# Kernel optimization log

Hardware: AMD Instinct MI355X
Metric: run time of the kernel (lower is better)

## Reference

```python
import jax, jax.numpy as jnp
import numpy as np
import math

PS = 8  # patch size (hard-coded in module)
DEPTH = 6
LAMBDA_INIT = 0.8 - 0.6 * math.exp(-0.3 * DEPTH)

# torch_dct norm=None DCT-II matrix: y_k = 2 * sum_n x_n cos(pi*(2n+1)k/(2N))
_n = np.arange(PS)
_C = 2.0 * np.cos(np.pi * (2 * _n[None, :] + 1) * _n[:, None] / (2 * PS))  # [k, n]
_Ci = np.linalg.inv(_C)
DCT_M = jnp.asarray(_C, jnp.float32)
IDCT_M = jnp.asarray(_Ci, jnp.float32)


def dct2(x):  # 2D DCT over last two dims (torch_dct.dct_2d, norm=None)
    return jnp.einsum('...mn,am,bn->...ab', x, DCT_M, DCT_M)


def idct2(x):  # exact inverse (torch_dct.idct_2d, norm=None)
    return jnp.einsum('...ab,ma,nb->...mn', x, IDCT_M, IDCT_M)


def conv1x1(x, w):  # w: [O, I]
    return jnp.einsum('oi,bihw->bohw', w, x)


def dw3(x, w):  # depthwise 3x3, stride 1, pad 1; w: [C, 1, 3, 3]
    return jax.lax.conv_general_dilated(
        x, w, window_strides=(1, 1), padding='SAME',
        dimension_numbers=('NCHW', 'OIHW', 'NCHW'),
        feature_group_count=x.shape[1])


def prelu(t, a):
    return jnp.where(t >= 0, t, a * t)


def setup_inputs() -> dict:
    key = jax.random.key(0)
    ks = jax.random.split(key, 20)
    b, c, H, W = 2, 64, 384, 384
    w = lambda k, shape: jax.random.normal(k, shape, jnp.float32) * 0.05
    heads = c // 16
    return {
        'x': jax.random.normal(ks[0], (b, c, H, W), jnp.float32),
        'nir': jax.random.normal(ks[1], (b, c, H, W), jnp.float32),
        'w_hidden': w(ks[2], (c, c)),
        'w_hidden_nir': w(ks[3], (2 * c, c)),
        'w_dw': w(ks[4], (c, 1, 3, 3)),
        'w_dw_nir': w(ks[5], (2 * c, 1, 3, 3)),
        'temperature': jnp.ones((heads, 1, 1), jnp.float32),
        'w_proj_mid': w(ks[6], (c, c)),
        'w_proj_out': w(ks[7], (c, c)),
        'w_p1a': w(ks[8], (c, 1, 3, 3)),
        'a_p1': jnp.asarray(0.25, jnp.float32),
        'w_p1b': w(ks[9], (c, 1, 3, 3)),
        'w_p2a': w(ks[10], (c, 1, 3, 3)),
        'a_p2': jnp.asarray(0.25, jnp.float32),
        'w_p2b': w(ks[11], (c, 1, 3, 3)),
        'lq1': jax.random.normal(ks[12], (c,), jnp.float32) * 0.1,
        'lk1': jax.random.normal(ks[13], (c,), jnp.float32) * 0.1,
        'lq2': jax.random.normal(ks[14], (c,), jnp.float32) * 0.1,
        'lk2': jax.random.normal(ks[15], (c,), jnp.float32) * 0.1,
    }


def reference(x, nir, w_hidden, w_hidden_nir, w_dw, w_dw_nir, temperature,
              w_proj_mid, w_proj_out, w_p1a, a_p1, w_p1b, w_p2a, a_p2, w_p2b,
              lq1, lk1, lq2, lk2):
    b, c, H, W = x.shape
    heads = c // 16
    hh, ww = H // PS, W // PS

    hidden = conv1x1(x, w_hidden)
    nir_hidden = conv1x1(nir, w_hidden_nir)
    q = dw3(hidden, w_dw)
    kv = dw3(nir_hidden, w_dw_nir)
    k, v = kv[:, :c], kv[:, c:]

    # b c (hh p1) (ww p2) -> b c hh ww p1 p2
    patch = lambda t: t.reshape(b, c, hh, PS, ww, PS).transpose(0, 1, 2, 4, 3, 5)
    q_fft = dct2(patch(q))
    k_fft = dct2(patch(k))
    out1 = q_fft * k_fft

    L = hh * ww * PS * PS
    hf = lambda t: t.reshape(b, heads, c // heads, L)  # b head c L
    q_fft, k_fft, out1f = hf(q_fft), hf(k_fft), hf(out1)

    qn = q_fft / jnp.maximum(jnp.linalg.norm(q_fft, axis=-1, keepdims=True), 1e-12)
    kn = k_fft / jnp.maximum(jnp.linalg.norm(k_fft, axis=-1, keepdims=True), 1e-12)

    attn = jax.nn.softmax(jnp.einsum('bhcl,bhdl->bhcd', qn, kn) * temperature, axis=-1)
    o = jnp.einsum('bhcd,bhdl->bhcl', attn, out1f)

    o = o.reshape(b, c, hh, ww, PS, PS)
    o = idct2(o)
    o = o.transpose(0, 1, 2, 4, 3, 5).reshape(b, c, H, W)
    out = conv1x1(o, w_proj_mid)

    lam1 = jnp.exp(jnp.sum(lq1 * lk1))
    lam2 = jnp.exp(jnp.sum(lq2 * lk2))
    lam = lam1 - lam2 + LAMBDA_INIT

    pool = lambda t, wa, a, wb: dw3(prelu(dw3(t, wa), a), wb)
    output = pool(q * out, w_p1a, a_p1, w_p1b) + pool(v - lam * (v * out), w_p2a, a_p2, w_p2b)
    return conv1x1(output, w_proj_out)
```

## Files before the change

kernel.cpp:

```cpp
#include <hip/hip_runtime.h>
#include <cmath>

#ifndef M_PI
#define M_PI 3.14159265358979323846
#endif

#define NB      2
#define N_PIX   147456
#define L_LEN   147456
#define TENS_SZ ((long)NB * 64 * N_PIX)

#define OFF_C    0
#define OFF_CI   64
#define OFF_LAM  128
#define OFF_GRAM 256
#define OFF_QQ   2304
#define OFF_KK   2432
#define OFF_ATTN 2560

#define TW 128
#define TH 16
#define LW 136
#define LH 18
#define PLH 20

__global__ __launch_bounds__(64) void init_k(const float* __restrict__ lq1, const float* __restrict__ lk1,
                                             const float* __restrict__ lq2, const float* __restrict__ lk2,
                                             float* __restrict__ sm) {
  int t = threadIdx.x;
  int a = t >> 3, m = t & 7;
  double cv = 2.0 * cos(M_PI * (double)((2 * m + 1) * a) / 16.0);
  sm[OFF_C + a * 8 + m] = (float)cv;
  sm[OFF_CI + m * 8 + a] = (float)(cv / ((a == 0) ? 32.0 : 16.0));
  float p1 = lq1[t] * lk1[t];
  float p2 = lq2[t] * lk2[t];
  #pragma unroll
  for (int off = 32; off; off >>= 1) {
    p1 += __shfl_xor(p1, off, 64);
    p2 += __shfl_xor(p2, off, 64);
  }
  if (t == 0) sm[OFF_LAM] = expf(p1) - expf(p2) + 0.70082066706704813f;
  for (int i = t; i < 2304; i += 64) sm[OFF_GRAM + i] = 0.f;
}

__global__ void diag_k(float* out, float v) { out[0] = v; }

__global__ __launch_bounds__(256) void conv1x1_k(const float* __restrict__ in, const float* __restrict__ w,
                                                 float* __restrict__ out) {
  __shared__ float ws[4096];
  int t = threadIdx.x;
  for (int j = t; j < 1024; j += 256)
    *reinterpret_cast<float4*>(ws + j * 4) = *reinterpret_cast<const float4*>(w + j * 4);
  __syncthreads();

  long gp = (long)blockIdx.x * 256;
  int bb = (int)(gp / N_PIX);
  int p0 = (int)(gp - (long)bb * N_PIX);
  int lane = t & 63;
  int co0 = (t >> 6) * 16;

  const float* ip = in + (long)bb * 64 * N_PIX + p0 + lane * 4;
  const float* wp = ws + co0 * 64;

  float acc[16][4];
  #pragma unroll
  for (int j = 0; j < 16; j++)
    #pragma unroll
    for (int p = 0; p < 4; p++) acc[j][p] = 0.f;

  for (int c4 = 0; c4 < 16; c4++) {
    float4 x0 = *reinterpret_cast<const float4*>(ip + (long)(c4 * 4 + 0) * N_PIX);
    float4 x1 = *reinterpret_cast<const float4*>(ip + (long)(c4 * 4 + 1) * N_PIX);
    float4 x2 = *reinterpret_cast<const float4*>(ip + (long)(c4 * 4 + 2) * N_PIX);
    float4 x3 = *reinterpret_cast<const float4*>(ip + (long)(c4 * 4 + 3) * N_PIX);
    #pragma unroll
    for (int j = 0; j < 16; j++) {
      float4 w4 = *reinterpret_cast<const float4*>(wp + j * 64 + c4 * 4);
// ... 41 lines not shown
    __syncthreads();
    const float* wp = ws + co0 * 64;
    float acc[16][4];
    #pragma unroll
    for (int j = 0; j < 16; j++)
      #pragma unroll
      for (int p = 0; p < 4; p++) acc[j][p] = 0.f;
    for (int c4 = 0; c4 < 16; c4++) {
      float4 x0 = *reinterpret_cast<const float4*>(ip + (long)(c4 * 4 + 0) * N_PIX);
      float4 x1 = *reinterpret_cast<const float4*>(ip + (long)(c4 * 4 + 1) * N_PIX);
      float4 x2 = *reinterpret_cast<const float4*>(ip + (long)(c4 * 4 + 2) * N_PIX);
      float4 x3 = *reinterpret_cast<const float4*>(ip + (long)(c4 * 4 + 3) * N_PIX);
      #pragma unroll
      for (int j = 0; j < 16; j++) {
        float4 w4 = *reinterpret_cast<const float4*>(wp + j * 64 + c4 * 4);
        acc[j][0] = fmaf(w4.x, x0.x, acc[j][0]);
        acc[j][0] = fmaf(w4.y, x1.x, acc[j][0]);
        acc[j][0] = fmaf(w4.z, x2.x, acc[j][0]);
        acc[j][0] = fmaf(w4.w, x3.x, acc[j][0]);
        acc[j][1] = fmaf(w4.x, x0.y, acc[j][1]);
        acc[j][1] = fmaf(w4.y, x1.y, acc[j][1]);
        acc[j][1] = fmaf(w4.z, x2.y, acc[j][1]);
        acc[j][1] = fmaf(w4.w, x3.y, acc[j][1]);
        acc[j][2] = fmaf(w4.x, x0.z, acc[j][2]);
        acc[j][2] = fmaf(w4.y, x1.z, acc[j][2]);
        acc[j][2] = fmaf(w4.z, x2.z, acc[j][2]);
        acc[j][2] = fmaf(w4.w, x3.z, acc[j][2]);
        acc[j][3] = fmaf(w4.x, x0.w, acc[j][3]);
        acc[j][3] = fmaf(w4.y, x1.w, acc[j][3]);
        acc[j][3] = fmaf(w4.z, x2.w, acc[j][3]);
        acc[j][3] = fmaf(w4.w, x3.w, acc[j][3]);
      }
    }
    float* op = (half ? outv : outk) + (long)bb * 64 * N_PIX + p0 + lane * 4;
    #pragma unroll
    for (int j = 0; j < 16; j++)
      *reinterpret_cast<float4*>(op + (long)(co0 + j) * N_PIX) =
          make_float4(acc[j][0], acc[j][1], acc[j][2], acc[j][3]);
  }
}

__device__ __forceinline__ float4 load_g4(const float* __restrict__ p, int gy, int gx) {
  if ((unsigned)gy >= 384u) return make_float4(0.f, 0.f, 0.f, 0.f);
  if (gx >= 0 && gx + 3 < 384) return *reinterpret_cast<const float4*>(p + gy * 384 + gx);
  float e[4];
  #pragma unroll
  for (int i = 0; i < 4; i++) {
    int xx = gx + i;
    e[i] = ((unsigned)xx < 384u) ? p[gy * 384 + xx] : 0.f;
  }
  return make_float4(e[0], e[1], e[2], e[3]);
}

__global__ __launch_bounds__(256) void dw3t_k(const float* __restrict__ in, const float* __restrict__ w,
                                              float* __restrict__ out) {
  __shared__ float sT[LH * LW];
  int plane = blockIdx.z;
  int ch = plane & 63;
  int x0 = blockIdx.x * TW, y0 = blockIdx.y * TH;
  const float* ip = in + (long)plane * N_PIX;
  int t = threadIdx.x;
  for (int j = t; j < LH * 34; j += 256) {
    int row = j / 34, c4 = j - row * 34;
    *reinterpret_cast<float4*>(sT + row * LW + c4 * 4) = load_g4(ip, y0 - 1 + row, x0 - 4 + c4 * 4);
  }
  __syncthreads();
  const float* wp = w + ch * 9;
  float w00 = wp[0], w01 = wp[1], w02 = wp[2];
  float w10 = wp[3], w11 = wp[4], w12 = wp[5];
  float w20 = wp[6], w21 = wp[7], w22 = wp[8];
  int col = t & 127, rg = t >> 7;
  int lc = col + 4;
  int r0 = rg * 8;
  float a0 = sT[r0 * LW + lc - 1],       a1 = sT[r0 * LW + lc],       a2 = sT[r0 * LW + lc + 1];
  float b0 = sT[(r0 + 1) * LW + lc - 1], b1 = sT[(r0 + 1) * LW + lc], b2 = sT[(r0 + 1) * LW + lc + 1];
  float* op = out + (long)plane * N_PIX + (long)(y0 + rg * 8) * 384 + x0 + col;
  #pragma unroll
  for (int i = 0; i < 8; i++) {
    int lr = r0 + i + 2;
    float c0 = sT[lr * LW + lc - 1], c1 = sT[lr * LW + lc], c2 = sT[lr * LW + lc + 1];
    float s = w00 * a0;
    s = fmaf(w01, a1, s); s = fmaf(w02, a2, s);
    s = fmaf(w10, b0, s); s = fmaf(w11, b1, s); s = fmaf(w12, b2, s);
    s = fmaf(w20, c0, s); s = fmaf(w21, c1, s); s = fmaf(w22, c2, s);
    op[i * 384] = s;
    a0 = b0; a1 = b1; a2 = b2;
    b0 = c0; b1 = c1; b2 = c2;
  }
}

__global__ __launch_bounds__(256) void dw3dct_k(const float* __restrict__ in, const float* __restrict__ w,
                                                const float* __restrict__ sm,
                                                float* __restrict__ outf, float* __restrict__ outs) {
  __shared__ float sT[LH * LW];
  __shared__ float Cm[64];
  int t = threadIdx.x;
  if (t < 64) Cm[t] = sm[OFF_C + t];
  int plane = blockIdx.z;
  int ch = plane & 63;
  int x0 = blockIdx.x * TW, y0 = blockIdx.y * TH;
  const float* ip = in + (long)plane * N_PIX;
  for (int j = t; j < LH * 34; j += 256) {
    int row = j / 34, c4 = j - row * 34;
    *reinterpret_cast<float4*>(sT + row * LW + c4 * 4) = load_g4(ip, y0 - 1 + row, x0 - 4 + c4 * 4);
  }
  __syncthreads();
  const float* wp = w + ch * 9;
  float w00 = wp[0], w01 = wp[1], w02 = wp[2];
  float w10 = wp[3], w11 = wp[4], w12 = wp[5];
  float w20 = wp[6], w21 = wp[7], w22 = wp[8];
  int col = t & 127, rg = t >> 7;
  int lc = col + 4;
  int r0 = rg * 8;
  float r[8];
  {
    float a0 = sT[r0 * LW + lc - 1],       a1 = sT[r0 * LW + lc],       a2 = sT[r0 * LW + lc + 1];
    float b0 = sT[(r0 + 1) * LW + lc - 1], b1 = sT[(r0 + 1) * LW + lc], b2 = sT[(r0 + 1) * LW + lc + 1];
    #pragma unroll
    for (int i = 0; i < 8; i++) {
      int lr = r0 + i + 2;
      float c0 = sT[lr * LW + lc - 1], c1 = sT[lr * LW + lc], c2 = sT[lr * LW + lc + 1];
      float s = w00 * a0;
      s = fmaf(w01, a1, s); s = fmaf(w02, a2, s);
      s = fmaf(w10, b0, s); s = fmaf(w11, b1, s); s = fmaf(w12, b2, s);
      s = fmaf(w20, c0, s); s = fmaf(w21, c1, s); s = fmaf(w22, c2, s);
      r[i] = s;
      a0 = b0; a1 = b1; a2 = b2;
      b0 = c0; b1 = c1; b2 = c2;
    }
  }
  if (outs) {
    float* op = outs + (long)plane * N_PIX + (long)(y0 + r0) * 384 + x0 + col;
    #pragma unroll
    for (int i = 0; i < 8; i++) op[i * 384] = r[i];
  }
  __syncthreads();
  #pragma unroll
  for (int i = 0; i < 8; i++) sT[(r0 + i + 1) * LW + lc] = r[i];
  __syncthreads();
  int patch = t >> 3, a = t & 7;
  int prow = patch >> 4, pcol = patch & 15;
  const float* xb = sT + (prow * 8 + 1) * LW + pcol * 8 + 4;
  float T[8];
  #pragma unroll
  for (int n = 0; n < 8; n++) {
    float s = 0.f;
    #pragma unroll
    for (int m = 0; m < 8; m++) s = fmaf(Cm[a * 8 + m], xb[m * LW + n], s);
    T[n] = s;
  }
  float o[8];
  #pragma unroll
  for (int b8 = 0; b8 < 8; b8++) {
    float s = 0.f;
    #pragma unroll
    for (int n = 0; n < 8; n++) s = fmaf(Cm[b8 * 8 + n], T[n], s);
    o[b8] = s;
  }
  int py = (y0 >> 3) + prow, px = (x0 >> 3) + pcol;
  float* op = outf + (long)plane * L_LEN + (long)(py * 48 + px) * 64 + a * 8;
  *reinterpret_cast<float4*>(op)     = make_float4(o[0], o[1], o[2], o[3]);
  *reinterpret_cast<float4*>(op + 4) = make_float4(o[4], o[5], o[6], o[7]);
}

__device__ __forceinline__ void stencil_col9(const float* __restrict__ sb, int ci, int rs0,
                                             float w00, float w01, float w02,
                                             float w10, float w11, float w12,
                                             float w20, float w21, float w22,
                                             float alpha, bool xok, int y0,
                                             float* __restrict__ r) {
  float a0 = sb[rs0 * LW + ci - 1],       a1 = sb[rs0 * LW + ci],       a2 = sb[rs0 * LW + ci + 1];
  float b0 = sb[(rs0 + 1) * LW + ci - 1], b1 = sb[(rs0 + 1) * LW + ci], b2 = sb[(rs0 + 1) * LW + ci + 1];
  #pragma unroll
  for (int ii = 0; ii < 9; ii++) {
    int rs2 = rs0 + ii + 2;
    float c0 = sb[rs2 * LW + ci - 1], c1 = sb[rs2 * LW + ci], c2 = sb[rs2 * LW + ci + 1];
    float s = w00 * a0;
    s = fmaf(w01, a1, s); s = fmaf(w02, a2, s);
    s = fmaf(w10, b0, s); s = fmaf(w11, b1, s); s = fmaf(w12, b2, s);
    s = fmaf(w20, c0, s); s = fmaf(w21, c1, s); s = fmaf(w22, c2, s);
    s = (s >= 0.f) ? s : alpha * s;
    int gy = y0 - 1 + rs0 + ii;
    r[ii] = (xok && (unsigned)gy < 384u) ? s : 0.f;
    a0 = b0; a1 = b1; a2 = b2;
    b0 = c0; b1 = c1; b2 = c2;
  }
}

__global__ __launch_bounds__(256) void pool_k(const float* __restrict__ q, const float* __restrict__ om,
                                              const float* __restrict__ v,
                                              const float* __restrict__ w1a, const float* __restrict__ a1p,
                                              const float* __restrict__ w1b,
                                              const float* __restrict__ w2a, const float* __restrict__ a2p,
                                              const float* __restrict__ w2b,
                                              const float* __restrict__ sm,
                                              float* __restrict__ outp) {
  __shared__ float s1[PLH * LW], s2[PLH * LW];
  int plane = blockIdx.z;
  int ch = plane & 63;
  int x0 = blockIdx.x * TW, y0 = blockIdx.y * TH;
  const float* qp = q  + (long)plane * N_PIX;
  const float* op = om + (long)plane * N_PIX;
  const float* vp = v  + (long)plane * N_PIX;
  float lam = sm[OFF_LAM];
  int t = threadIdx.x;
  for (int j = t; j < PLH * 34; j += 256) {
    int row = j / 34, c4 = j - row * 34;
    int gy = y0 - 2 + row, gx = x0 - 4 + c4 * 4;
    float4 qv = load_g4(qp, gy, gx);
    float4 ov = load_g4(op, gy, gx);
    float4 vv = load_g4(vp, gy, gx);
    *reinterpret_cast<float4*>(s1 + row * LW + c4 * 4) =
        make_float4(qv.x * ov.x, qv.y * ov.y, qv.z * ov.z, qv.w * ov.w);
    *reinterpret_cast<float4*>(s2 + row * LW + c4 * 4) =
        make_float4(vv.x - lam * vv.x * ov.x, vv.y - lam * vv.y * ov.y,
                    vv.z - lam * vv.z * ov.z, vv.w - lam * vv.w * ov.w);
  }
  __syncthreads();

  int ct = t & 127, rg = t >> 7;
  int rs0 = rg * 9;
  int ci0 = 3 + ct;
  int ci1 = 131 + ct;
  bool xok0 = (unsigned)(x0 - 4 + ci0) < 384u;
  bool xok1 = (unsigned)(x0 - 4 + ci1) < 384u;

  {
    const float* wp1 = w1a + ch * 9;
    float w00 = wp1[0], w01 = wp1[1], w02 = wp1[2], w10 = wp1[3], w11 = wp1[4],
          w12 = wp1[5], w20 = wp1[6], w21 = wp1[7], w22 = wp1[8];
    float alpha = a1p[0];
    float rm[9], re[9];
    stencil_col9(s1, ci0, rs0, w00, w01, w02, w10, w11, w12, w20, w21, w22, alpha, xok0, y0, rm);
    if (ct < 2)
      stencil_col9(s1, ci1, rs0, w00, w01, w02, w10, w11, w12, w20, w21, w22, alpha, xok1, y0, re);
    __syncthreads();
    #pragma unroll
    for (int ii = 0; ii < 9; ii++) s1[(rs0 + ii + 1) * LW + ci0] = rm[ii];
    if (ct < 2) {
      #pragma unroll
      for (int ii = 0; ii < 9; ii++) s1[(rs0 + ii + 1) * LW + ci1] = re[ii];
    }
  }
  {
    const float* wp2 = w2a + ch * 9;
    float w00 = wp2[0], w01 = wp2[1], w02 = wp2[2], w10 = wp2[3], w11 = wp2[4],
          w12 = wp2[5], w20 = wp2[6], w21 = wp2[7], w22 = wp2[8];
    float alpha = a2p[0];
    float rm[9], re[9];
    stencil_col9(s2, ci0, rs0, w00, w01, w02, w10, w11, w12, w20, w21, w22, alpha, xok0, y0, rm);
    if (ct < 2)
      stencil_col9(s2, ci1, rs0, w00, w01, w02, w10, w11, w12, w20, w21, w22, alpha, xok1, y0, re);
    __syncthreads();
    #pragma unroll
    for (int ii = 0; ii < 9; ii++) s2[(rs0 + ii + 1) * LW + ci0] = rm[ii];
    if (ct < 2) {
      #pragma unroll
      for (int ii = 0; ii < 9; ii++) s2[(rs0 + ii + 1) * LW + ci1] = re[ii];
    }
  }
  __syncthreads();
  {
    const float* wp1 = w1b + ch * 9;
    const float* wp2 = w2b + ch * 9;
    float p00 = wp1[0], p01 = wp1[1], p02 = wp1[2], p10 = wp1[3], p11 = wp1[4], p12 = wp1[5], p20 = wp1[6], p21 = wp1[7], p22 = wp1[8];
    float q00 = wp2[0], q01 = wp2[1], q02 = wp2[2], q10 = wp2[3], q11 = wp2[4], q12 = wp2[5], q20 = wp2[6], q21 = wp2[7], q22 = wp2[8];
    int col = t & 127, rg2 = t >> 7;
    int lc = col + 4;
    int rb = rg2 * 8 + 1;
    float xa0 = s1[rb * LW + lc - 1],       xa1 = s1[rb * LW + lc],       xa2 = s1[rb * LW + lc + 1];
    float xb0 = s1[(rb + 1) * LW + lc - 1], xb1 = s1[(rb + 1) * LW + lc], xb2 = s1[(rb + 1) * LW + lc + 1];
    float ya0 = s2[rb * LW + lc - 1],       ya1 = s2[rb * LW + lc],       ya2 = s2[rb * LW + lc + 1];
    float yb0 = s2[(rb + 1) * LW + lc - 1], yb1 = s2[(rb + 1) * LW + lc], yb2 = s2[(rb + 1) * LW + lc + 1];
    float* wo = outp + (long)plane * N_PIX + (long)(y0 + rg2 * 8) * 384 + x0 + col;
    #pragma unroll
    for (int i = 0; i < 8; i++) {
      int lr = rb + i + 2;
      float xc0 = s1[lr * LW + lc - 1], xc1 = s1[lr * LW + lc], xc2 = s1[lr * LW + lc + 1];
      float yc0 = s2[lr * LW + lc - 1], yc1 = s2[lr * LW + lc], yc2 = s2[lr * LW + lc + 1];
      float s = p00 * xa0;
      s = fmaf(p01, xa1, s); s = fmaf(p02, xa2, s);
      s = fmaf(p10, xb0, s); s = fmaf(p11, xb1, s); s = fmaf(p12, xb2, s);
      s = fmaf(p20, xc0, s); s = fmaf(p21, xc1, s); s = fmaf(p22, xc2, s);
      s = fmaf(q00, ya0, s); s = fmaf(q01, ya1, s); s = fmaf(q02, ya2, s);
      s = fmaf(q10, yb0, s); s = fmaf(q11, yb1, s); s = fmaf(q12, yb2, s);
      s = fmaf(q20, yc0, s); s = fmaf(q21, yc1, s); s = fmaf(q22, yc2, s);
      wo[i * 384] = s;
      xa0 = xb0; xa1 = xb1; xa2 = xb2; xb0 = xc0; xb1 = xc1; xb2 = xc2;
      ya0 = yb0; ya1 = yb1; ya2 = yb2; yb0 = yc0; yb1 = yc1; yb2 = yc2;
    }
  }
}

__global__ __launch_bounds__(256) void dct_k(const float* __restrict__ in,
                                             const float* __restrict__ sm, float* __restrict__ outf) {
  __shared__ float Cm[64];
  if (threadIdx.x < 64) Cm[threadIdx.x] = sm[OFF_C + threadIdx.x];
  __syncthreads();
  int pid = blockIdx.x * 256 + threadIdx.x;
  int wx = pid % 48;
  int t1 = pid / 48;
  int hy = t1 % 48; t1 /= 48;
  int ch = t1 & 63;
  int bb = t1 >> 6;
  const float* ip = in + (long)(bb * 64 + ch) * N_PIX + (hy * 8) * 384 + wx * 8;
  float X[8][8];
  #pragma unroll
  for (int r = 0; r < 8; r++) {
    float4 v0 = *reinterpret_cast<const float4*>(ip + r * 384);
    float4 v1 = *reinterpret_cast<const float4*>(ip + r * 384 + 4);
    X[r][0] = v0.x; X[r][1] = v0.y; X[r][2] = v0.z; X[r][3] = v0.w;
    X[r][4] = v1.x; X[r][5] = v1.y; X[r][6] = v1.z; X[r][7] = v1.w;
  }
  float T[8][8];
  #pragma unroll
  for (int a = 0; a < 8; a++)
    #pragma unroll
    for (int n = 0; n < 8; n++) {
      float s = 0.f;
      #pragma unroll
      for (int m = 0; m < 8; m++) s = fmaf(Cm[a * 8 + m], X[m][n], s);
      T[a][n] = s;
    }
  #pragma unroll
  for (int a = 0; a < 8; a++)
    #pragma unroll
    for (int b8 = 0; b8 < 8; b8++) {
      float s = 0.f;
      #pragma unroll
      for (int n = 0; n < 8; n++) s = fmaf(Cm[b8 * 8 + n], T[a][n], s);
      X[a][b8] = s;
    }
  float* op = outf + (long)(bb * 64 + ch) * L_LEN + (long)(hy * 48 + wx) * 64;
  float4* o4 = reinterpret_cast<float4*>(op);
  #pragma unroll
  for (int a = 0; a < 8; a++) {
    o4[a * 2]     = make_float4(X[a][0], X[a][1], X[a][2], X[a][3]);
    o4[a * 2 + 1] = make_float4(X[a][4], X[a][5], X[a][6], X[a][7]);
  }
}

#define GS_P 132
__global__ __launch_bounds__(256) void gram_k(const float* __restrict__ qf, const float* __restrict__ kf,
                                              float* __restrict__ sm) {
  __shared__ float qs[16 * GS_P], ks[16 * GS_P];
  int t = threadIdx.x;
  int bh = blockIdx.y;
  int bb = bh >> 2, h = bh & 3;
  const float* qbase = qf + ((long)bb * 64 + h * 16) * L_LEN;
  const float* kbase = kf + ((long)bb * 64 + h * 16) * L_LEN;
  int c = t >> 4, d = t & 15;
  long l0 = (long)blockIdx.x * 2048;
  float g = 0.f, nq = 0.f, nk = 0.f;
  for (int chunk = 0; chunk < 16; chunk++) {
    long lc = l0 + chunk * 128;
    __syncthreads();
    for (int j = t; j < 512; j += 256) {
      int row = j >> 5, c4 = j & 31;
      *reinterpret_cast<float4*>(qs + row * GS_P + c4 * 4) =
          *reinterpret_cast<const float4*>(qbase + (long)row * L_LEN + lc + c4 * 4);
      *reinterpret_cast<float4*>(ks + row * GS_P + c4 * 4) =
          *reinterpret_cast<const float4*>(kbase + (long)row * L_LEN + lc + c4 * 4);
    }
    __syncthreads();
    #pragma unroll
    for (int i = 0; i < 128; i += 4) {
      float4 a = *reinterpret_cast<const float4*>(qs + c * GS_P + i);
      float4 b = *reinterpret_cast<const float4*>(ks + d * GS_P + i);
      g  = fmaf(a.x, b.x, g);  g  = fmaf(a.y, b.y, g);  g  = fmaf(a.z, b.z, g);  g  = fmaf(a.w, b.w, g);
      nq = fmaf(a.x, a.x, nq); nq = fmaf(a.y, a.y, nq); nq = fmaf(a.z, a.z, nq); nq = fmaf(a.w, a.w, nq);
      nk = fmaf(b.x, b.x, nk); nk = fmaf(b.y, b.y, nk); nk = fmaf(b.z, b.z, nk); nk = fmaf(b.w, b.w, nk);
    }
  }
  atomicAdd(&sm[OFF_GRAM + bh * 256 + c * 16 + d], g);
  if (d == 0) atomicAdd(&sm[OFF_QQ + bh * 16 + c], nq);
  if (c == 0) atomicAdd(&sm[OFF_KK + bh * 16 + d], nk);
}

__global__ __launch_bounds__(256) void attn_k(const float* __restrict__ temp, float* __restrict__ sm) {
  int bh = blockIdx.x;
  int h = bh & 3;
  int t = threadIdx.x;
  int c = t >> 4, d = t & 15;
  float qn = fmaxf(sqrtf(sm[OFF_QQ + bh * 16 + c]), 1e-12f);
  float kn = fmaxf(sqrtf(sm[OFF_KK + bh * 16 + d]), 1e-12f);
  float v = sm[OFF_GRAM + bh * 256 + t] / (qn * kn) * temp[h];
  float mx = v;
  #pragma unroll
  for (int o = 8; o; o >>= 1) mx = fmaxf(mx, __shfl_xor(mx, o, 16));
  float e = expf(v - mx);
  float s = e;
  #pragma unroll
  for (int o = 8; o; o >>= 1) s += __shfl_xor(s, o, 16);
  sm[OFF_ATTN + bh * 256 + t] = e / s;
}

#define CB_P 273
__global__ __launch_bounds__(256) void comb_idct_k(const float* __restrict__ qf, const float* __restrict__ kf,
                                                   const float* __restrict__ sm, float* __restrict__ out) {
  __shared__ float A[256];
  __shared__ float Ci[64];
  __shared__ float sb[16 * CB_P];
  int bh = blockIdx.y;
  int t = threadIdx.x;
  A[t] = sm[OFF_ATTN + bh * 256 + t];
  if (t < 64) Ci[t] = sm[OFF_CI + t];
  __syncthreads();
  int bb = bh >> 2, h = bh & 3;
  long l = (long)blockIdx.x * 256 + t;
  const float* qp = qf + ((long)bb * 64 + h * 16) * L_LEN + l;
  const float* kp = kf + ((long)bb * 64 + h * 16) * L_LEN + l;
  float p[16];
  #pragma unroll
  for (int d = 0; d < 16; d++) p[d] = qp[(long)d * L_LEN] * kp[(long)d * L_LEN];
  int pl_w = t >> 6, i_w = t & 63;
  #pragma unroll
  for (int c = 0; c < 16; c++) {
    float s = 0.f;
    #pragma unroll
    for (int d = 0; d < 16; d++) s = fmaf(A[c * 16 + d], p[d], s);
    sb[c * CB_P + pl_w * 68 + i_w] = s;
  }
  __syncthreads();
  int j = t & 3, c = (t >> 2) & 15, pl = t >> 6;
  const float* fb = sb + c * CB_P + pl * 68;
  float F[8][8];
  #pragma unroll
  for (int a = 0; a < 8; a++)
    #pragma unroll
    for (int b8 = 0; b8 < 8; b8++) F[a][b8] = fb[a * 8 + b8];
  int patch = blockIdx.x * 4 + pl;
  int hy = patch / 48, wx = patch - hy * 48;
  float* op = out + ((long)bb * 64 + h * 16 + c) * N_PIX + (long)(hy * 8) * 384 + wx * 8;
  #pragma unroll
  for (int mm = 0; mm < 2; mm++) {
    int m = 2 * j + mm;
    float T[8];
    #pragma unroll
    for (int b8 = 0; b8 < 8; b8++) {
      float s = 0.f;
      #pragma unroll
      for (int a = 0; a < 8; a++) s = fmaf(Ci[m * 8 + a], F[a][b8], s);
      T[b8] = s;
    }
    float o[8];
    #pragma unroll
    for (int n = 0; n < 8; n++) {
      float s = 0.f;
      #pragma unroll
      for (int b8 = 0; b8 < 8; b8++) s = fmaf(Ci[n * 8 + b8], T[b8], s);
      o[n] = s;
    }
    *reinterpret_cast<float4*>(op + m * 384)     = make_float4(o[0], o[1], o[2], o[3]);
    *reinterpret_cast<float4*>(op + m * 384 + 4) = make_float4(o[4], o[5], o[6], o[7]);
  }
}

__global__ __launch_bounds__(256) void combine_k(float* __restrict__ qf, const float* __restrict__ kf,
                                                 const float* __restrict__ sm) {
  __shared__ float A[256];
  int bh = blockIdx.y;
  A[threadIdx.x] = sm[OFF_ATTN + bh * 256 + threadIdx.x];
  __syncthreads();
  int bb = bh >> 2, h = bh & 3;
  long l = (long)blockIdx.x * 256 + threadIdx.x;
  float* qp = qf + ((long)bb * 64 + h * 16) * L_LEN + l;
  const float* kp = kf + ((long)bb * 64 + h * 16) * L_LEN + l;
  float p[16];
  #pragma unroll
  for (int d = 0; d < 16; d++) p[d] = qp[(long)d * L_LEN] * kp[(long)d * L_LEN];
  #pragma unroll
  for (int c = 0; c < 16; c++) {
    float s = 0.f;
    #pragma unroll
    for (int d = 0; d < 16; d++) s = fmaf(A[c * 16 + d], p[d], s);
    qp[(long)c * L_LEN] = s;
  }
}

__global__ __launch_bounds__(256) void idct_k(const float* __restrict__ inf, const float* __restrict__ sm,
                                              float* __restrict__ out) {
  __shared__ float Ci[64];
  if (threadIdx.x < 64) Ci[threadIdx.x] = sm[OFF_CI + threadIdx.x];
  __syncthreads();
  int pid = blockIdx.x * 256 + threadIdx.x;
  int wx = pid % 48;
  int t1 = pid / 48;
  int hy = t1 % 48; t1 /= 48;
  int ch = t1 & 63;
  int bb = t1 >> 6;
  const float4* i4 = reinterpret_cast<const float4*>(inf + (long)(bb * 64 + ch) * L_LEN + (long)(hy * 48 + wx) * 64);
  float F[8][8];
  #pragma unroll
  for (int a = 0; a < 8; a++) {
    float4 v0 = i4[a * 2], v1 = i4[a * 2 + 1];
    F[a][0] = v0.x; F[a][1] = v0.y; F[a][2] = v0.z; F[a][3] = v0.w;
    F[a][4] = v1.x; F[a][5] = v1.y; F[a][6] = v1.z; F[a][7] = v1.w;
  }
  float T[8][8];
  #pragma unroll
  for (int m = 0; m < 8; m++)
    #pragma unroll
    for (int b8 = 0; b8 < 8; b8++) {
      float s = 0.f;
      #pragma unroll
      for (int a = 0; a < 8; a++) s = fmaf(Ci[m * 8 + a], F[a][b8], s);
      T[m][b8] = s;
    }
  #pragma unroll
  for (int m = 0; m < 8; m++)
    #pragma unroll
    for (int n = 0; n < 8; n++) {
      float s = 0.f;
      #pragma unroll
      for (int b8 = 0; b8 < 8; b8++) s = fmaf(Ci[n * 8 + b8], T[m][b8], s);
      F[m][n] = s;
    }
  float* op = out + (long)(bb * 64 + ch) * N_PIX + (hy * 8) * 384 + wx * 8;
  #pragma unroll
  for (int m = 0; m < 8; m++) {
    *reinterpret_cast<float4*>(op + m * 384)     = make_float4(F[m][0], F[m][1], F[m][2], F[m][3]);
    *reinterpret_cast<float4*>(op + m * 384 + 4) = make_float4(F[m][4], F[m][5], F[m][6], F[m][7]);
  }
}

extern "C" void kernel_launch(void* const* d_in, const int* in_sizes, int n_in,
                              void* d_out, int out_size, void* d_ws, size_t ws_size,
                              hipStream_t stream) {
  const float* x            = (const float*)d_in[0];
  const float* nir          = (const float*)d_in[1];
  const float* w_hidden     = (const float*)d_in[2];
  const float* w_hidden_nir = (const float*)d_in[3];
  const float* w_dw         = (const float*)d_in[4];
  const float* w_dw_nir     = (const float*)d_in[5];
  const float* temperature  = (const float*)d_in[6];
  const float* w_proj_mid   = (const float*)d_in[7];
  const float* w_proj_out   = (const float*)d_in[8];
  const float* w_p1a        = (const float*)d_in[9];
  const float* a_p1         = (const float*)d_in[10];
  const float* w_p1b        = (const float*)d_in[11];
  const float* w_p2a        = (const float*)d_in[12];
  const float* a_p2         = (const float*)d_in[13];
  const float* w_p2b        = (const float*)d_in[14];
  const float* lq1          = (const float*)d_in[15];
  const float* lk1          = (const float*)d_in[16];
  const float* lq2          = (const float*)d_in[17];
  const float* lk2          = (const float*)d_in[18];

  float* OUT = (float*)d_out;
  float* W0 = (float*)d_ws;
  float* W1 = W0 + TENS_SZ;
  float* W2 = W1 + TENS_SZ;
  float* SM = W2 + TENS_SZ;
  float* W3 = SM + 8192;

  size_t needed3 = (size_t)3 * TENS_SZ * sizeof(float) + 32768;
  size_t needed4 = ((size_t)4 * TENS_SZ + 8192) * sizeof(float);
  if (ws_size < needed3) {
    diag_k<<<1, 1, 0, stream>>>(OUT, 1000.0f + (float)(ws_size >> 20));
    return;
  }
  bool big = ws_size >= needed4;

  dim3 blk256(256);
  dim3 gridST(3, 24, NB * 64);

  init_k<<<1, 64, 0, stream>>>(lq1, lk1, lq2, lk2, SM);

  if (big) {
    conv1x1_nir2_k<<<1152, blk256, 0, stream>>>(nir, w_hidden_nir, W0, W1);
    dw3t_k<<<gridST, blk256, 0, stream>>>(W1, w_dw_nir + 64 * 9, W2);
    dw3dct_k<<<gridST, blk256, 0, stream>>>(W0, w_dw_nir, SM, W1, nullptr);
    conv1x1_k<<<1152, blk256, 0, stream>>>(x, w_hidden, W0);
    dw3dct_k<<<gridST, blk256, 0, stream>>>(W0, w_dw, SM, W3, OUT);
    gram_k<<<dim3(72, 8), blk256, 0, stream>>>(W3, W1, SM);
    attn_k<<<8, blk256, 0, stream>>>(temperature, SM);
    comb_idct_k<<<dim3(576, 8), blk256, 0, stream>>>(W3, W1, SM, W0);
    conv1x1_k<<<1152, blk256, 0, stream>>>(W0, w_proj_mid, W1);
    pool_k<<<gridST, blk256, 0, stream>>>(OUT, W1, W2, w_p1a, a_p1, w_p1b, w_p2a, a_p2, w_p2b, SM, W3);
    conv1x1_k<<<1152, blk256, 0, stream>>>(W3, w_proj_out, OUT);
  } else {
    conv1x1_k<<<1152, blk256, 0, stream>>>(x, w_hidden, W0);
    dw3t_k<<<gridST, blk256, 0, stream>>>(W0, w_dw, OUT);
    conv1x1_k<<<1152, blk256, 0, stream>>>(nir, w_hidden_nir, W0);
    dw3t_k<<<gridST, blk256, 0, stream>>>(W0, w_dw_nir, W1);
    conv1x1_k<<<1152, blk256, 0, stream>>>(nir, w_hidden_nir + 64 * 64, W0);
    dw3t_k<<<gridST, blk256, 0, stream>>>(W0, w_dw_nir + 64 * 9, W2);
    dct_k<<<1152, blk256, 0, stream>>>(W1, SM, W0);
    dct_k<<<1152, blk256, 0, stream>>>(OUT, SM, W1);
    gram_k<<<dim3(72, 8), blk256, 0, stream>>>(W1, W0, SM);
    attn_k<<<8, blk256, 0, stream>>>(temperature, SM);
    combine_k<<<dim3(576, 8), blk256, 0, stream>>>(W1, W0, SM);
    idct_k<<<1152, blk256, 0, stream>>>(W1, SM, W0);
    conv1x1_k<<<1152, blk256, 0, stream>>>(W0, w_proj_mid, W1);
    pool_k<<<gridST, blk256, 0, stream>>>(OUT, W1, W2, w_p1a, a_p1, w_p1b, w_p2a, a_p2, w_p2b, SM, W0);
    conv1x1_k<<<1152, blk256, 0, stream>>>(W0, w_proj_out, OUT);
  }
}
```

Before: 751.2 us.

## Recompute q and v depthwise convs inside pool kernel and fuse q*k product into gram

After: 712.0 us. 1.06x faster.

```diff
diff --git a/kernel.cpp b/kernel.cpp
--- a/kernel.cpp
+++ b/kernel.cpp
@@ -22,7 +22,7 @@
 #define TH 16
 #define LW 136
 #define LH 18
-#define PLH 20
+#define PVH 22
 
 __global__ __launch_bounds__(64) void init_k(const float* __restrict__ lq1, const float* __restrict__ lk1,
                                              const float* __restrict__ lq2, const float* __restrict__ lk2,
@@ -170,46 +170,9 @@
   return make_float4(e[0], e[1], e[2], e[3]);
 }
 
-__global__ __launch_bounds__(256) void dw3t_k(const float* __restrict__ in, const float* __restrict__ w,
-                                              float* __restrict__ out) {
-  __shared__ float sT[LH * LW];
-  int plane = blockIdx.z;
-  int ch = plane & 63;
-  int x0 = blockIdx.x * TW, y0 = blockIdx.y * TH;
-  const float* ip = in + (long)plane * N_PIX;
-  int t = threadIdx.x;
-  for (int j = t; j < LH * 34; j += 256) {
-    int row = j / 34, c4 = j - row * 34;
-    *reinterpret_cast<float4*>(sT + row * LW + c4 * 4) = load_g4(ip, y0 - 1 + row, x0 - 4 + c4 * 4);
-  }
-  __syncthreads();
-  const float* wp = w + ch * 9;
-  float w00 = wp[0], w01 = wp[1], w02 = wp[2];
-  float w10 = wp[3], w11 = wp[4], w12 = wp[5];
-  float w20 = wp[6], w21 = wp[7], w22 = wp[8];
-  int col = t & 127, rg = t >> 7;
-  int lc = col + 4;
-  int r0 = rg * 8;
-  float a0 = sT[r0 * LW + lc - 1],       a1 = sT[r0 * LW + lc],       a2 = sT[r0 * LW + lc + 1];
-  float b0 = sT[(r0 + 1) * LW + lc - 1], b1 = sT[(r0 + 1) * LW + lc], b2 = sT[(r0 + 1) * LW + lc + 1];
-  float* op = out + (long)plane * N_PIX + (long)(y0 + rg * 8) * 384 + x0 + col;
-  #pragma unroll
-  for (int i = 0; i < 8; i++) {
-    int lr = r0 + i + 2;
-    float c0 = sT[lr * LW + lc - 1], c1 = sT[lr * LW + lc], c2 = sT[lr * LW + lc + 1];
-    float s = w00 * a0;
-    s = fmaf(w01, a1, s); s = fmaf(w02, a2, s);
-    s = fmaf(w10, b0, s); s = fmaf(w11, b1, s); s = fmaf(w12, b2, s);
-    s = fmaf(w20, c0, s); s = fmaf(w21, c1, s); s = fmaf(w22, c2, s);
-    op[i * 384] = s;
-    a0 = b0; a1 = b1; a2 = b2;
-    b0 = c0; b1 = c1; b2 = c2;
-  }
-}
-
 __global__ __launch_bounds__(256) void dw3dct_k(const float* __restrict__ in, const float* __restrict__ w,
                                                 const float* __restrict__ sm,
-                                                float* __restrict__ outf, float* __restrict__ outs) {
+                                                float* __restrict__ outf) {
   __shared__ float sT[LH * LW];
   __shared__ float Cm[64];
   int t = threadIdx.x;
@@ -246,11 +209,6 @@
       a0 = b0; a1 = b1; a2 = b2;
       b0 = c0; b1 = c1; b2 = c2;
     }
-  }
-  if (outs) {
-    float* op = outs + (long)plane * N_PIX + (long)(y0 + r0) * 384 + x0 + col;
-    #pragma unroll
-    for (int i = 0; i < 8; i++) op[i * 384] = r[i];
   }
   __syncthreads();
   #pragma unroll
@@ -305,76 +263,147 @@
   }
 }
 
-__global__ __launch_bounds__(256) void pool_k(const float* __restrict__ q, const float* __restrict__ om,
-                                              const float* __restrict__ v,
-                                              const float* __restrict__ w1a, const float* __restrict__ a1p,
-                                              const float* __restrict__ w1b,
-                                              const float* __restrict__ w2a, const float* __restrict__ a2p,
-                                              const float* __restrict__ w2b,
-                                              const float* __restrict__ sm,
-                                              float* __restrict__ outp) {
-  __shared__ float s1[PLH * LW], s2[PLH * LW];
+__device__ __forceinline__ void dw3_col10(const float* __restrict__ sb, int ci, int rs0,
+                                          float w00, float w01, float w02,
+                                          float w10, float w11, float w12,
+                                          float w20, float w21, float w22,
+                                          float* __restrict__ r) {
+  float a0 = sb[rs0 * LW + ci - 1],       a1 = sb[rs0 * LW + ci],       a2 = sb[rs0 * LW + ci + 1];
+  float b0 = sb[(rs0 + 1) * LW + ci - 1], b1 = sb[(rs0 + 1) * LW + ci], b2 = sb[(rs0 + 1) * LW + ci + 1];
+  #pragma unroll
+  for (int ii = 0; ii < 10; ii++) {
+    int rs2 = rs0 + ii + 2;
+    float c0 = sb[rs2 * LW + ci - 1], c1 = sb[rs2 * LW + ci], c2 = sb[rs2 * LW + ci + 1];
+    float s = w00 * a0;
+    s = fmaf(w01, a1, s); s = fmaf(w02, a2, s);
+    s = fmaf(w10, b0, s); s = fmaf(w11, b1, s); s = fmaf(w12, b2, s);
+    s = fmaf(w20, c0, s); s = fmaf(w21, c1, s); s = fmaf(w22, c2, s);
+    r[ii] = s;
+    a0 = b0; a1 = b1; a2 = b2;
+    b0 = c0; b1 = c1; b2 = c2;
+  }
+}
+
+__global__ __launch_bounds__(256) void pool3_k(const float* __restrict__ hidden, const float* __restrict__ vpre,
+                                               const float* __restrict__ om,
+                                               const float* __restrict__ wq, const float* __restrict__ wv,
+                                               const float* __restrict__ w1a, const float* __restrict__ a1p,
+                                               const float* __restrict__ w1b,
+                                               const float* __restrict__ w2a, const float* __restrict__ a2p,
+                                               const float* __restrict__ w2b,
+                                               const float* __restrict__ sm,
+                                               float* __restrict__ outp) {
+  __shared__ float s1[PVH * LW], s2[PVH * LW];
   int plane = blockIdx.z;
   int ch = plane & 63;
   int x0 = blockIdx.x * TW, y0 = blockIdx.y * TH;
-  const float* qp = q  + (long)plane * N_PIX;
-  const float* op = om + (long)plane * N_PIX;
-  const float* vp = v  + (long)plane * N_PIX;
+  const float* hp = hidden + (long)plane * N_PIX;
+  const float* vp = vpre + (long)plane * N_PIX;
+  const float* op_ = om + (long)plane * N_PIX;
   float lam = sm[OFF_LAM];
   int t = threadIdx.x;
-  for (int j = t; j < PLH * 34; j += 256) {
+  for (int j = t; j < PVH * 34; j += 256) {
     int row = j / 34, c4 = j - row * 34;
-    int gy = y0 - 2 + row, gx = x0 - 4 + c4 * 4;
-    float4 qv = load_g4(qp, gy, gx);
-    float4 ov = load_g4(op, gy, gx);
-    float4 vv = load_g4(vp, gy, gx);
-    *reinterpret_cast<float4*>(s1 + row * LW + c4 * 4) =
-        make_float4(qv.x * ov.x, qv.y * ov.y, qv.z * ov.z, qv.w * ov.w);
-    *reinterpret_cast<float4*>(s2 + row * LW + c4 * 4) =
-        make_float4(vv.x - lam * vv.x * ov.x, vv.y - lam * vv.y * ov.y,
-                    vv.z - lam * vv.z * ov.z, vv.w - lam * vv.w * ov.w);
+    int gy = y0 - 3 + row, gx = x0 - 4 + c4 * 4;
+    *reinterpret_cast<float4*>(s1 + row * LW + c4 * 4) = load_g4(hp, gy, gx);
+    *reinterpret_cast<float4*>(s2 + row * LW + c4 * 4) = load_g4(vp, gy, gx);
   }
   __syncthreads();
 
   int ct = t & 127, rg = t >> 7;
+  int rsV = rg * 10;
+  int ciV0 = 2 + ct;
+  int ciV1 = 130 + ct;
+  float p1m[10], p1e[10], p2m[10], p2e[10];
+  {
+    const float* wp = wq + ch * 9;
+    float w00 = wp[0], w01 = wp[1], w02 = wp[2], w10 = wp[3], w11 = wp[4],
+          w12 = wp[5], w20 = wp[6], w21 = wp[7], w22 = wp[8];
+    dw3_col10(s1, ciV0, rsV, w00, w01, w02, w10, w11, w12, w20, w21, w22, p1m);
+    if (ct < 4)
+      dw3_col10(s1, ciV1, rsV, w00, w01, w02, w10, w11, w12, w20, w21, w22, p1e);
+  }
+  {
+    const float* wp = wv + ch * 9;
+    float w00 = wp[0], w01 = wp[1], w02 = wp[2], w10 = wp[3], w11 = wp[4],
+          w12 = wp[5], w20 = wp[6], w21 = wp[7], w22 = wp[8];
+    dw3_col10(s2, ciV0, rsV, w00, w01, w02, w10, w11, w12, w20, w21, w22, p2m);
+    if (ct < 4)
+      dw3_col10(s2, ciV1, rsV, w00, w01, w02, w10, w11, w12, w20, w21, w22, p2e);
+  }
+  {
+    int gx0 = x0 - 4 + ciV0, gx1 = x0 - 4 + ciV1;
+    bool vx0 = (unsigned)gx0 < 384u, vx1 = (unsigned)gx1 < 384u;
+    #pragma unroll
+    for (int ii = 0; ii < 10; ii++) {
+      int gy = y0 - 2 + rsV + ii;
+      bool oky = (unsigned)gy < 384u;
+      if (oky && vx0) {
+        float o = op_[gy * 384 + gx0];
+        p1m[ii] = p1m[ii] * o;
+        float vv = p2m[ii];
+        p2m[ii] = vv - lam * vv * o;
+      } else { p1m[ii] = 0.f; p2m[ii] = 0.f; }
+      if (ct < 4) {
+        if (oky && vx1) {
+          float o = op_[gy * 384 + gx1];
+          p1e[ii] = p1e[ii] * o;
+          float vv = p2e[ii];
+          p2e[ii] = vv - lam * vv * o;
+        } else { p1e[ii] = 0.f; p2e[ii] = 0.f; }
+      }
+    }
+  }
+  __syncthreads();
+  #pragma unroll
+  for (int ii = 0; ii < 10; ii++) {
+    s1[(rsV + 1 + ii) * LW + ciV0] = p1m[ii];
+    s2[(rsV + 1 + ii) * LW + ciV0] = p2m[ii];
+  }
+  if (ct < 4) {
+    #pragma unroll
+    for (int ii = 0; ii < 10; ii++) {
+      s1[(rsV + 1 + ii) * LW + ciV1] = p1e[ii];
+      s2[(rsV + 1 + ii) * LW + ciV1] = p2e[ii];
+    }
+  }
+  __syncthreads();
+  float* s1p = s1 + LW;
+  float* s2p = s2 + LW;
   int rs0 = rg * 9;
-  int ci0 = 3 + ct;
-  int ci1 = 131 + ct;
+  int ci0 = 3 + ct, ci1 = 131 + ct;
   bool xok0 = (unsigned)(x0 - 4 + ci0) < 384u;
   bool xok1 = (unsigned)(x0 - 4 + ci1) < 384u;
-
+  float u1m[9], u1e[9], u2m[9], u2e[9];
   {
     const float* wp1 = w1a + ch * 9;
     float w00 = wp1[0], w01 = wp1[1], w02 = wp1[2], w10 = wp1[3], w11 = wp1[4],
           w12 = wp1[5], w20 = wp1[6], w21 = wp1[7], w22 = wp1[8];
     float alpha = a1p[0];
-    float rm[9], re[9];
-    stencil_col9(s1, ci0, rs0, w00, w01, w02, w10, w11, w12, w20, w21, w22, alpha, xok0, y0, rm);
+    stencil_col9(s1p, ci0, rs0, w00, w01, w02, w10, w11, w12, w20, w21, w22, alpha, xok0, y0, u1m);
     if (ct < 2)
-      stencil_col9(s1, ci1, rs0, w00, w01, w02, w10, w11, w12, w20, w21, w22, alpha, xok1, y0, re);
-    __syncthreads();
-    #pragma unroll
-    for (int ii = 0; ii < 9; ii++) s1[(rs0 + ii + 1) * LW + ci0] = rm[ii];
-    if (ct < 2) {
-      #pragma unroll
-      for (int ii = 0; ii < 9; ii++) s1[(rs0 + ii + 1) * LW + ci1] = re[ii];
-    }
+      stencil_col9(s1p, ci1, rs0, w00, w01, w02, w10, w11, w12, w20, w21, w22, alpha, xok1, y0, u1e);
   }
   {
     const float* wp2 = w2a + ch * 9;
     float w00 = wp2[0], w01 = wp2[1], w02 = wp2[2], w10 = wp2[3], w11 = wp2[4],
           w12 = wp2[5], w20 = wp2[6], w21 = wp2[7], w22 = wp2[8];
     float alpha = a2p[0];
-    float rm[9], re[9];
-    stencil_col9(s2, ci0, rs0, w00, w01, w02, w10, w11, w12, w20, w21, w22, alpha, xok0, y0, rm);
+    stencil_col9(s2p, ci0, rs0, w00, w01, w02, w10, w11, w12, w20, w21, w22, alpha, xok0, y0, u2m);
     if (ct < 2)
-      stencil_col9(s2, ci1, rs0, w00, w01, w02, w10, w11, w12, w20, w21, w22, alpha, xok1, y0, re);
-    __syncthreads();
-    #pragma unroll
-    for (int ii = 0; ii < 9; ii++) s2[(rs0 + ii + 1) * LW + ci0] = rm[ii];
-    if (ct < 2) {
-      #pragma unroll
-      for (int ii = 0; ii < 9; ii++) s2[(rs0 + ii + 1) * LW + ci1] = re[ii];
+      stencil_col9(s2p, ci1, rs0, w00, w01, w02, w10, w11, w12, w20, w21, w22, alpha, xok1, y0, u2e);
+  }
+  __syncthreads();
+  #pragma unroll
+  for (int ii = 0; ii < 9; ii++) {
+    s1p[(rs0 + ii + 1) * LW + ci0] = u1m[ii];
+    s2p[(rs0 + ii + 1) * LW + ci0] = u2m[ii];
+  }
+  if (ct < 2) {
+    #pragma unroll
+    for (int ii = 0; ii < 9; ii++) {
+      s1p[(rs0 + ii + 1) * LW + ci1] = u1e[ii];
+      s2p[(rs0 + ii + 1) * LW + ci1] = u2e[ii];
     }
   }
   __syncthreads();
@@ -386,16 +415,16 @@
     int col = t & 127, rg2 = t >> 7;
     int lc = col + 4;
     int rb = rg2 * 8 + 1;
-    float xa0 = s1[rb * LW + lc - 1],       xa1 = s1[rb * LW + lc],       xa2 = s1[rb * LW + lc + 1];
-    float xb0 = s1[(rb + 1) * LW + lc - 1], xb1 = s1[(rb + 1) * LW + lc], xb2 = s1[(rb + 1) * LW + lc + 1];
-    float ya0 = s2[rb * LW + lc - 1],       ya1 = s2[rb * LW + lc],       ya2 = s2[rb * LW + lc + 1];
-    float yb0 = s2[(rb + 1) * LW + lc - 1], yb1 = s2[(rb + 1) * LW + lc], yb2 = s2[(rb + 1) * LW + lc + 1];
+    float xa0 = s1p[rb * LW + lc - 1],       xa1 = s1p[rb * LW + lc],       xa2 = s1p[rb * LW + lc + 1];
+    float xb0 = s1p[(rb + 1) * LW + lc - 1], xb1 = s1p[(rb + 1) * LW + lc], xb2 = s1p[(rb + 1) * LW + lc + 1];
+    float ya0 = s2p[rb * LW + lc - 1],       ya1 = s2p[rb * LW + lc],       ya2 = s2p[rb * LW + lc + 1];
+    float yb0 = s2p[(rb + 1) * LW + lc - 1], yb1 = s2p[(rb + 1) * LW + lc], yb2 = s2p[(rb + 1) * LW + lc + 1];
     float* wo = outp + (long)plane * N_PIX + (long)(y0 + rg2 * 8) * 384 + x0 + col;
     #pragma unroll
     for (int i = 0; i < 8; i++) {
       int lr = rb + i + 2;
-      float xc0 = s1[lr * LW + lc - 1], xc1 = s1[lr * LW + lc], xc2 = s1[lr * LW + lc + 1];
-      float yc0 = s2[lr * LW + lc - 1], yc1 = s2[lr * LW + lc], yc2 = s2[lr * LW + lc + 1];
+      float xc0 = s1p[lr * LW + lc - 1], xc1 = s1p[lr * LW + lc], xc2 = s1p[lr * LW + lc + 1];
+      float yc0 = s2p[lr * LW + lc - 1], yc1 = s2p[lr * LW + lc], yc2 = s2p[lr * LW + lc + 1];
       float s = p00 * xa0;
       s = fmaf(p01, xa1, s); s = fmaf(p02, xa2, s);
       s = fmaf(p10, xb0, s); s = fmaf(p11, xb1, s); s = fmaf(p12, xb2, s);
@@ -410,63 +439,15 @@
   }
 }
 
-__global__ __launch_bounds__(256) void dct_k(const float* __restrict__ in,
-                                             const float* __restrict__ sm, float* __restrict__ outf) {
-  __shared__ float Cm[64];
-  if (threadIdx.x < 64) Cm[threadIdx.x] = sm[OFF_C + threadIdx.x];
-  __syncthreads();
-  int pid = blockIdx.x * 256 + threadIdx.x;
-  int wx = pid % 48;
-  int t1 = pid / 48;
-  int hy = t1 % 48; t1 /= 48;
-  int ch = t1 & 63;
-  int bb = t1 >> 6;
-  const float* ip = in + (long)(bb * 64 + ch) * N_PIX + (hy * 8) * 384 + wx * 8;
-  float X[8][8];
-  #pragma unroll
-  for (int r = 0; r < 8; r++) {
-    float4 v0 = *reinterpret_cast<const float4*>(ip + r * 384);
-    float4 v1 = *reinterpret_cast<const float4*>(ip + r * 384 + 4);
-    X[r][0] = v0.x; X[r][1] = v0.y; X[r][2] = v0.z; X[r][3] = v0.w;
-    X[r][4] = v1.x; X[r][5] = v1.y; X[r][6] = v1.z; X[r][7] = v1.w;
-  }
-  float T[8][8];
-  #pragma unroll
-  for (int a = 0; a < 8; a++)
-    #pragma unroll
-    for (int n = 0; n < 8; n++) {
-      float s = 0.f;
-      #pragma unroll
-      for (int m = 0; m < 8; m++) s = fmaf(Cm[a * 8 + m], X[m][n], s);
-      T[a][n] = s;
-    }
-  #pragma unroll
-  for (int a = 0; a < 8; a++)
-    #pragma unroll
-    for (int b8 = 0; b8 < 8; b8++) {
-      float s = 0.f;
-      #pragma unroll
-      for (int n = 0; n < 8; n++) s = fmaf(Cm[b8 * 8 + n], T[a][n], s);
-      X[a][b8] = s;
-    }
-  float* op = outf + (long)(bb * 64 + ch) * L_LEN + (long)(hy * 48 + wx) * 64;
-  float4* o4 = reinterpret_cast<float4*>(op);
-  #pragma unroll
-  for (int a = 0; a < 8; a++) {
-    o4[a * 2]     = make_float4(X[a][0], X[a][1], X[a][2], X[a][3]);
-    o4[a * 2 + 1] = make_float4(X[a][4], X[a][5], X[a][6], X[a][7]);
-  }
-}
-
 #define GS_P 132
-__global__ __launch_bounds__(256) void gram_k(const float* __restrict__ qf, const float* __restrict__ kf,
+__global__ __launch_bounds__(256) void gram_k(const float* __restrict__ qf, float* __restrict__ kf,
                                               float* __restrict__ sm) {
   __shared__ float qs[16 * GS_P], ks[16 * GS_P];
   int t = threadIdx.x;
   int bh = blockIdx.y;
   int bb = bh >> 2, h = bh & 3;
   const float* qbase = qf + ((long)bb * 64 + h * 16) * L_LEN;
-  const float* kbase = kf + ((long)bb * 64 + h * 16) * L_LEN;
+  float* kbase = kf + ((long)bb * 64 + h * 16) * L_LEN;
   int c = t >> 4, d = t & 15;
   long l0 = (long)blockIdx.x * 2048;
   float g = 0.f, nq = 0.f, nk = 0.f;
@@ -475,10 +456,12 @@
     __syncthreads();
     for (int j = t; j < 512; j += 256) {
       int row = j >> 5, c4 = j & 31;
-      *reinterpret_cast<float4*>(qs + row * GS_P + c4 * 4) =
-          *reinterpret_cast<const float4*>(qbase + (long)row * L_LEN + lc + c4 * 4);
-      *reinterpret_cast<float4*>(ks + row * GS_P + c4 * 4) =
-          *reinterpret_cast<const float4*>(kbase + (long)row * L_LEN + lc + c4 * 4);
+      float4 qv = *reinterpret_cast<const float4*>(qbase + (long)row * L_LEN + lc + c4 * 4);
+      float4 kv = *reinterpret_cast<const float4*>(kbase + (long)row * L_LEN + lc + c4 * 4);
+      *reinterpret_cast<float4*>(qs + row * GS_P + c4 * 4) = qv;
+      *reinterpret_cast<float4*>(ks + row * GS_P + c4 * 4) = kv;
+      *reinterpret_cast<float4*>(kbase + (long)row * L_LEN + lc + c4 * 4) =
+          make_float4(qv.x * kv.x, qv.y * kv.y, qv.z * kv.z, qv.w * kv.w);
     }
     __syncthreads();
     #pragma unroll
@@ -514,7 +497,7 @@
 }
 
 #define CB_P 273
-__global__ __launch_bounds__(256) void comb_idct_k(const float* __restrict__ qf, const float* __restrict__ kf,
+__global__ __launch_bounds__(256) void comb_idct_k(const float* __restrict__ of,
                                                    const float* __restrict__ sm, float* __restrict__ out) {
   __shared__ float A[256];
   __shared__ float Ci[64];
@@ -526,11 +509,10 @@
   __syncthreads();
   int bb = bh >> 2, h = bh & 3;
   long l = (long)blockIdx.x * 256 + t;
-  const float* qp = qf + ((long)bb * 64 + h * 16) * L_LEN + l;
-  const float* kp = kf + ((long)bb * 64 + h * 16) * L_LEN + l;
+  const float* kp = of + ((long)bb * 64 + h * 16) * L_LEN + l;
   float p[16];
   #pragma unroll
-  for (int d = 0; d < 16; d++) p[d] = qp[(long)d * L_LEN] * kp[(long)d * L_LEN];
+  for (int d = 0; d < 16; d++) p[d] = kp[(long)d * L_LEN];
   int pl_w = t >> 6, i_w = t & 63;
   #pragma unroll
   for (int c = 0; c < 16; c++) {
@@ -571,74 +553,6 @@
     }
     *reinterpret_cast<float4*>(op + m * 384)     = make_float4(o[0], o[1], o[2], o[3]);
     *reinterpret_cast<float4*>(op + m * 384 + 4) = make_float4(o[4], o[5], o[6], o[7]);
-  }
-}
-
-__global__ __launch_bounds__(256) void combine_k(float* __restrict__ qf, const float* __restrict__ kf,
-                                                 const float* __restrict__ sm) {
-  __shared__ float A[256];
-  int bh = blockIdx.y;
-  A[threadIdx.x] = sm[OFF_ATTN + bh * 256 + threadIdx.x];
-  __syncthreads();
-  int bb = bh >> 2, h = bh & 3;
-  long l = (long)blockIdx.x * 256 + threadIdx.x;
-  float* qp = qf + ((long)bb * 64 + h * 16) * L_LEN + l;
-  const float* kp = kf + ((long)bb * 64 + h * 16) * L_LEN + l;
-  float p[16];
-  #pragma unroll
-  for (int d = 0; d < 16; d++) p[d] = qp[(long)d * L_LEN] * kp[(long)d * L_LEN];
-  #pragma unroll
-  for (int c = 0; c < 16; c++) {
-    float s = 0.f;
-    #pragma unroll
-    for (int d = 0; d < 16; d++) s = fmaf(A[c * 16 + d], p[d], s);
-    qp[(long)c * L_LEN] = s;
-  }
-}
-
-__global__ __launch_bounds__(256) void idct_k(const float* __restrict__ inf, const float* __restrict__ sm,
-                                              float* __restrict__ out) {
-  __shared__ float Ci[64];
-  if (threadIdx.x < 64) Ci[threadIdx.x] = sm[OFF_CI + threadIdx.x];
-  __syncthreads();
-  int pid = blockIdx.x * 256 + threadIdx.x;
-  int wx = pid % 48;
-  int t1 = pid / 48;
-  int hy = t1 % 48; t1 /= 48;
-  int ch = t1 & 63;
-  int bb = t1 >> 6;
-  const float4* i4 = reinterpret_cast<const float4*>(inf + (long)(bb * 64 + ch) * L_LEN + (long)(hy * 48 + wx) * 64);
-  float F[8][8];
-  #pragma unroll
-  for (int a = 0; a < 8; a++) {
-    float4 v0 = i4[a * 2], v1 = i4[a * 2 + 1];
-    F[a][0] = v0.x; F[a][1] = v0.y; F[a][2] = v0.z; F[a][3] = v0.w;
-    F[a][4] = v1.x; F[a][5] = v1.y; F[a][6] = v1.z; F[a][7] = v1.w;
-  }
-  float T[8][8];
-  #pragma unroll
-  for (int m = 0; m < 8; m++)
-    #pragma unroll
-    for (int b8 = 0; b8 < 8; b8++) {
-      float s = 0.f;
-      #pragma unroll
-      for (int a = 0; a < 8; a++) s = fmaf(Ci[m * 8 + a], F[a][b8], s);
-      T[m][b8] = s;
-    }
-  #pragma unroll
-  for (int m = 0; m < 8; m++)
-    #pragma unroll
-    for (int n = 0; n < 8; n++) {
-      float s = 0.f;
-      #pragma unroll
-      for (int b8 = 0; b8 < 8; b8++) s = fmaf(Ci[n * 8 + b8], T[m][b8], s);
-      F[m][n] = s;
-    }
-  float* op = out + (long)(bb * 64 + ch) * N_PIX + (hy * 8) * 384 + wx * 8;
-  #pragma unroll
-  for (int m = 0; m < 8; m++) {
-    *reinterpret_cast<float4*>(op + m * 384)     = make_float4(F[m][0], F[m][1], F[m][2], F[m][3]);
-    *reinterpret_cast<float4*>(op + m * 384 + 4) = make_float4(F[m][4], F[m][5], F[m][6], F[m][7]);
   }
 }
 
@@ -670,48 +584,26 @@
   float* W1 = W0 + TENS_SZ;
   float* W2 = W1 + TENS_SZ;
   float* SM = W2 + TENS_SZ;
-  float* W3 = SM + 8192;
-
-  size_t needed3 = (size_t)3 * TENS_SZ * sizeof(float) + 32768;
-  size_t needed4 = ((size_t)4 * TENS_SZ + 8192) * sizeof(float);
-  if (ws_size < needed3) {
+
+  size_t needed = (size_t)3 * TENS_SZ * sizeof(float) + 32768;
+  if (ws_size < needed) {
     diag_k<<<1, 1, 0, stream>>>(OUT, 1000.0f + (float)(ws_size >> 20));
     return;
   }
-  bool big = ws_size >= needed4;
 
   dim3 blk256(256);
   dim3 gridST(3, 24, NB * 64);
 
   init_k<<<1, 64, 0, stream>>>(lq1, lk1, lq2, lk2, SM);
-
-  if (big) {
-    conv1x1_nir2_k<<<1152, blk256, 0, stream>>>(nir, w_hidden_nir, W0, W1);
-    dw3t_k<<<gridST, blk256, 0, stream>>>(W1, w_dw_nir + 64 * 9, W2);
-    dw3dct_k<<<gridST, blk256, 0, stream>>>(W0, w_dw_nir, SM, W1, nullptr);
-    conv1x1_k<<<1152, blk256, 0, stream>>>(x, w_hidden, W0);
-    dw3dct_k<<<gridST, blk256, 0, stream>>>(W0, w_dw, SM, W3, OUT);
-    gram_k<<<dim3(72, 8), blk256, 0, stream>>>(W3, W1, SM);
-    attn_k<<<8, blk256, 0, stream>>>(temperature, SM);
-    comb_idct_k<<<dim3(576, 8), blk256, 0, stream>>>(W3, W1, SM, W0);
-    conv1x1_k<<<1152, blk256, 0, stream>>>(W0, w_proj_mid, W1);
-    pool_k<<<gridST, blk256, 0, stream>>>(OUT, W1, W2, w_p1a, a_p1, w_p1b, w_p2a, a_p2, w_p2b, SM, W3);
-    conv1x1_k<<<1152, blk256, 0, stream>>>(W3, w_proj_out, OUT);
-  } else {
-    conv1x1_k<<<1152, blk256, 0, stream>>>(x, w_hidden, W0);
-    dw3t_k<<<gridST, blk256, 0, stream>>>(W0, w_dw, OUT);
-    conv1x1_k<<<1152, blk256, 0, stream>>>(nir, w_hidden_nir, W0);
-    dw3t_k<<<gridST, blk256, 0, stream>>>(W0, w_dw_nir, W1);
-    conv1x1_k<<<1152, blk256, 0, stream>>>(nir, w_hidden_nir + 64 * 64, W0);
-    dw3t_k<<<gridST, blk256, 0, stream>>>(W0, w_dw_nir + 64 * 9, W2);
-    dct_k<<<1152, blk256, 0, stream>>>(W1, SM, W0);
-    dct_k<<<1152, blk256, 0, stream>>>(OUT, SM, W1);
-    gram_k<<<dim3(72, 8), blk256, 0, stream>>>(W1, W0, SM);
-    attn_k<<<8, blk256, 0, stream>>>(temperature, SM);
-    combine_k<<<dim3(576, 8), blk256, 0, stream>>>(W1, W0, SM);
-    idct_k<<<1152, blk256, 0, stream>>>(W1, SM, W0);
-    conv1x1_k<<<1152, blk256, 0, stream>>>(W0, w_proj_mid, W1);
-    pool_k<<<gridST, blk256, 0, stream>>>(OUT, W1, W2, w_p1a, a_p1, w_p1b, w_p2a, a_p2, w_p2b, SM, W0);
-    conv1x1_k<<<1152, blk256, 0, stream>>>(W0, w_proj_out, OUT);
-  }
-}
+  conv1x1_nir2_k<<<1152, blk256, 0, stream>>>(nir, w_hidden_nir, W2, W1);
+  dw3dct_k<<<gridST, blk256, 0, stream>>>(W2, w_dw_nir, SM, OUT);
+  conv1x1_k<<<1152, blk256, 0, stream>>>(x, w_hidden, W0);
+  dw3dct_k<<<gridST, blk256, 0, stream>>>(W0, w_dw, SM, W2);
+  gram_k<<<dim3(72, 8), blk256, 0, stream>>>(W2, OUT, SM);
+  attn_k<<<8, blk256, 0, stream>>>(temperature, SM);
+  comb_idct_k<<<dim3(576, 8), blk256, 0, stream>>>(OUT, SM, W2);
+  conv1x1_k<<<1152, blk256, 0, stream>>>(W2, w_proj_mid, OUT);
+  pool3_k<<<gridST, blk256, 0, stream>>>(W0, W1, OUT, w_dw, w_dw_nir + 64 * 9,
+                                         w_p1a, a_p1, w_p1b, w_p2a, a_p2, w_p2b, SM, W2);
+  conv1x1_k<<<1152, blk256, 0, stream>>>(W2, w_proj_out, OUT);
+}
```
